# Kernel optimization log

Hardware: AMD Instinct MI355X
Metric: run time of the kernel (lower is better)

Reference implementation:

```python
import jax, jax.numpy as jnp
import numpy as np

N, E = 10000, 160000
EPS = 1e-5  # BatchNorm eps (eval mode: running_mean=0, running_var=1)


def _bn(x, g, b):
    # eval-mode batchnorm with default running stats
    return g * x / np.float32(np.sqrt(1.0 + EPS)) + b


def _conv(x, w, b, stride, pad):
    y = jax.lax.conv_general_dilated(
        x, w, (stride, stride), [(pad, pad), (pad, pad)],
        dimension_numbers=('NCHW', 'OIHW', 'NCHW'))
    return y + b[None, :, None, None]


def _maxpool3(x):
    # kernel 3, stride 1, pad 1
    return jax.lax.reduce_window(x, -jnp.inf, jax.lax.max,
                                 (1, 1, 3, 3), (1, 1, 1, 1),
                                 [(0, 0), (0, 0), (1, 1), (1, 1)])


def _sage_conv(x, edge_index, wl, bl, wr):
    # PyG SAGEConv(aggr='mean'): out = lin_l(mean_j x_j) + lin_r(x_i)
    src, dst = edge_index[0], edge_index[1]
    n = x.shape[0]
    agg = jax.ops.segment_sum(x[src], dst, num_segments=n)
    cnt = jax.ops.segment_sum(jnp.ones((edge_index.shape[1],), x.dtype), dst, num_segments=n)
    agg = agg / jnp.maximum(cnt, 1.0)[:, None]
    return agg @ wl.T + bl + x @ wr.T


def setup_inputs():
    key = jax.random.key(0)
    ks = jax.random.split(key, 16)
    w = lambda k, shape, fan: jax.random.normal(k, shape, jnp.float32) / np.float32(np.sqrt(fan))
    return {
        'x': jax.random.normal(ks[0], (N, 2560), jnp.float32),
        'edge_index': jax.random.randint(ks[1], (2, E), 0, N),
        'w1l': w(ks[2], (1024, 2560), 2560), 'b1': jnp.zeros((1024,), jnp.float32),
        'w1r': w(ks[3], (1024, 2560), 2560),
        'bn1_g': jnp.ones((1024,), jnp.float32), 'bn1_b': jnp.zeros((1024,), jnp.float32),
        'w2l': w(ks[4], (512, 1024), 1024), 'b2': jnp.zeros((512,), jnp.float32),
        'w2r': w(ks[5], (512, 1024), 1024),
        'fa1_w': w(ks[6], (128, 512), 512), 'fa1_b': jnp.zeros((128,), jnp.float32),
        'fa2_w': w(ks[7], (128, 128), 128), 'fa2_b': jnp.zeros((128,), jnp.float32),
        'cnn1_w': w(ks[8], (64, 1, 3, 3), 9), 'cnn1_b': jnp.zeros((64,), jnp.float32),
        'norm_g': jnp.ones((64,), jnp.float32), 'norm_b': jnp.zeros((64,), jnp.float32),
        'c1_w': w(ks[9], (64, 64, 3, 3), 576), 'c1_b': jnp.zeros((64,), jnp.float32),
        'c1_g': jnp.ones((64,), jnp.float32), 'c1_bb': jnp.zeros((64,), jnp.float32),
        'c2_w': w(ks[10], (16, 64, 3, 3), 576), 'c2_b': jnp.zeros((16,), jnp.float32),
        'c2_g': jnp.ones((16,), jnp.float32), 'c2_bb': jnp.zeros((16,), jnp.float32),
        'fc1_w': w(ks[11], (1024, 432), 432), 'fc1_b': jnp.zeros((1024,), jnp.float32),
        'fc2_w': w(ks[12], (14, 1024), 1024), 'fc2_b': jnp.zeros((14,), jnp.float32),
    }


def reference(x, edge_index, w1l, b1, w1r, bn1_g, bn1_b, w2l, b2, w2r,
              fa1_w, fa1_b, fa2_w, fa2_b, cnn1_w, cnn1_b, norm_g, norm_b,
              c1_w, c1_b, c1_g, c1_bb, c2_w, c2_b, c2_g, c2_bb,
              fc1_w, fc1_b, fc2_w, fc2_b):
    # ---- SAGE (eval mode: dropout inactive) ----
    h = _sage_conv(x, edge_index, w1l, b1, w1r)
    h = jax.nn.relu(h)
    h = _bn(h, bn1_g, bn1_b)
    h = _sage_conv(h, edge_index, w2l, b2, w2r)      # [N, 512]
    xb = h[None]                                      # [1, N, 512]
    # ---- Attention pooling (softmax over node axis) ----
    a = jnp.tanh(xb @ fa1_w.T + fa1_b) @ fa2_w.T + fa2_b   # [1, N, 128]
    att = jax.nn.softmax(a, axis=1).transpose(0, 2, 1)     # [1, 128, N]
    emb = (att @ xb)[None]                                  # [1, 1, 128, 512]
    # ---- CNN classifier ----
    e = _conv(emb, cnn1_w, cnn1_b, 1, 3)                    # [1,64,132,516]
    e = jax.nn.relu(_bn(e, norm_g[None, :, None, None], norm_b[None, :, None, None]))
    for _ in range(5):
        e = _conv(e, c1_w, c1_b, 2, 1)
        e = jax.nn.relu(_bn(e, c1_g[None, :, None, None], c1_bb[None, :, None, None]))
        e = _maxpool3(e)
    e = _conv(e, c2_w, c2_b, 2, 1)                          # [1,16,3,9]
    e = jax.nn.relu(_bn(e, c2_g[None, :, None, None], c2_bb[None, :, None, None]))
    e = _maxpool3(e)
    e = e.reshape(e.shape[0], -1)                           # [1, 432]
    e = e @ fc1_w.T + fc1_b
    e = e @ fc2_w.T + fc2_b
    return jax.nn.sigmoid(e)                                # [1, 14]
```

## Files before the change

### kernel.cpp

```cpp
#include <hip/hip_runtime.h>
#include <cstdint>
#include <cstddef>

typedef unsigned short ushort;
typedef __attribute__((ext_vector_type(8))) short bf16x8;
typedef __attribute__((ext_vector_type(8))) unsigned short ushort8v;
typedef __attribute__((ext_vector_type(4))) float f32x4;

#define BN_INV 0.9999950000374997f

__device__ inline ushort f2bf(float f) {
    union { float f; unsigned u; } x; x.f = f;
    unsigned r = x.u + 0x7fffu + ((x.u >> 16) & 1u);
    return (ushort)(r >> 16);
}
__device__ inline float bf2f(ushort u) {
    union { unsigned u; float f; } x; x.u = ((unsigned)u) << 16;
    return x.f;
}

__device__ __forceinline__ void gload16(const void* g, void* l) {
    __builtin_amdgcn_global_load_lds(
        (const __attribute__((address_space(1))) unsigned int*)g,
        (__attribute__((address_space(3))) unsigned int*)l, 16, 0, 0);
// ... 97 lines not shown
            acc[3][3] = __builtin_amdgcn_mfma_f32_16x16x32_bf16(a3, b3, acc[3][3], 0, 0, 0);
        }
    }

#pragma unroll
    for (int mi = 0; mi < 4; mi++) {
#pragma unroll
        for (int ni = 0; ni < 4; ni++) {
            f32x4 a = acc[mi][ni];
            int n = n0 + wc * 64 + ni * 16 + lr;
#pragma unroll
            for (int j = 0; j < 4; j++) {
                int m = m0 + wr * 64 + mi * 16 + lg * 4 + j;
                if (m >= M) continue;
                float v = a[j];
                if (EPIL == 3) {
                    v = tanhf(v + bias[n]);
                } else if (EPIL == 4) {
                    v = v + bias[n];
                }
                if (EPIL == 5) {
                    int half = N >> 1;
                    ushort* dst = (n < half) ? (ushort*)C : C2;
                    dst[(size_t)m * half + (n & (half - 1))] = f2bf(v);
                } else {
                    if (sizeof(OutT) == 2) ((ushort*)C)[(size_t)m * N + n] = f2bf(v);
                    else                   ((float*)C)[(size_t)m * N + n] = v;
                }
            }
        }
    }
}

__global__ void gather_h1(const ushort* __restrict__ YL, const int* __restrict__ eidx,
                          const int* __restrict__ off, const ushort* __restrict__ YR,
// ... 36 lines not shown
        s0 += bf2f(v[0]); s1 += bf2f(v[1]); s2 += bf2f(v[2]); s3 += bf2f(v[3]);
        s4 += bf2f(v[4]); s5 += bf2f(v[5]); s6 += bf2f(v[6]); s7 += bf2f(v[7]);
    }
    float sv[8] = {s0, s1, s2, s3, s4, s5, s6, s7};
    ushort8v zr = *(const ushort8v*)(ZR + (size_t)n * 512 + threadIdx.x * 8);
    ushort8v o;
#pragma unroll
    for (int qq = 0; qq < 8; qq++) {
        int c = threadIdx.x * 8 + qq;
        o[qq] = f2bf(sv[qq] * inv + b2[c] + bf2f(zr[qq]));
    }
    *(ushort8v*)(XB + (size_t)n * 512 + threadIdx.x * 8) = o;
}

__global__ __launch_bounds__(256)
void mgemm_splitk(const ushort* __restrict__ Asrc, const ushort* __restrict__ Bsrc,
                  float* __restrict__ PART, int N, int Kp, int nsteps, int spz)
{
    __shared__ ushort As[128 * 64];
    __shared__ ushort Bs[128 * 64];

    const int tid  = threadIdx.x;
    const int lane = tid & 63;
    const int wid  = tid >> 6;
    const int wr   = wid >> 1;
    const int wc   = wid & 1;
    const int n0   = blockIdx.x * 128;
    const int z    = blockIdx.z;

    const int lr  = lane & 15;
    const int lg  = lane >> 4;
    const int swz = (lr & 7) << 4;

    f32x4 acc[4][4];
#pragma unroll
    for (int i = 0; i < 4; i++)
#pragma unroll
        for (int j = 0; j < 4; j++) acc[i][j] = (f32x4){0.f, 0.f, 0.f, 0.f};

    const int sb = z * spz;
    const int se = min(sb + spz, nsteps);

    for (int s = sb; s < se; s++) {
        int k0 = s * 64;
        if (s != sb) __syncthreads();
#pragma unroll
        for (int i = 0; i < 4; i++) {
            int ch = i * 256 + tid;
            int rr = ch >> 3, c8 = ch & 7;
            int c8p = c8 ^ (rr & 7);
            gload16(Asrc + (size_t)rr * Kp + k0 + c8p * 8,
                    (char*)As + (i * 256 + wid * 64) * 16);
            gload16(Bsrc + (size_t)(n0 + rr) * Kp + k0 + c8p * 8,
                    (char*)Bs + (i * 256 + wid * 64) * 16);
        }
        __syncthreads();

        const char* Ab = (const char*)As + (wr * 64 + lr) * 128;
        const char* Bb = (const char*)Bs + (wc * 64 + lr) * 128;
#pragma unroll
        for (int ks = 0; ks < 2; ks++) {
            int kx = (ks * 64 + lg * 16) ^ swz;
            bf16x8 a0 = *(const bf16x8*)(Ab + 0 * 2048 + kx);
            bf16x8 a1 = *(const bf16x8*)(Ab + 1 * 2048 + kx);
            bf16x8 a2 = *(const bf16x8*)(Ab + 2 * 2048 + kx);
            bf16x8 a3 = *(const bf16x8*)(Ab + 3 * 2048 + kx);
            bf16x8 b0 = *(const bf16x8*)(Bb + 0 * 2048 + kx);
            bf16x8 b1 = *(const bf16x8*)(Bb + 1 * 2048 + kx);
            bf16x8 b2 = *(const bf16x8*)(Bb + 2 * 2048 + kx);
            bf16x8 b3 = *(const bf16x8*)(Bb + 3 * 2048 + kx);
            acc[0][0] = __builtin_amdgcn_mfma_f32_16x16x32_bf16(a0, b0, acc[0][0], 0, 0, 0);
            acc[0][1] = __builtin_amdgcn_mfma_f32_16x16x32_bf16(a0, b1, acc[0][1], 0, 0, 0);
// ... 2 lines not shown
            acc[1][0] = __builtin_amdgcn_mfma_f32_16x16x32_bf16(a1, b0, acc[1][0], 0, 0, 0);
            acc[1][1] = __builtin_amdgcn_mfma_f32_16x16x32_bf16(a1, b1, acc[1][1], 0, 0, 0);
            acc[1][2] = __builtin_amdgcn_mfma_f32_16x16x32_bf16(a1, b2, acc[1][2], 0, 0, 0);
            acc[1][3] = __builtin_amdgcn_mfma_f32_16x16x32_bf16(a1, b3, acc[1][3], 0, 0, 0);
            acc[2][0] = __builtin_amdgcn_mfma_f32_16x16x32_bf16(a2, b0, acc[2][0], 0, 0, 0);
            acc[2][1] = __builtin_amdgcn_mfma_f32_16x16x32_bf16(a2, b1, acc[2][1], 0, 0, 0);
            acc[2][2] = __builtin_amdgcn_mfma_f32_16x16x32_bf16(a2, b2, acc[2][2], 0, 0, 0);
            acc[2][3] = __builtin_amdgcn_mfma_f32_16x16x32_bf16(a2, b3, acc[2][3], 0, 0, 0);
            acc[3][0] = __builtin_amdgcn_mfma_f32_16x16x32_bf16(a3, b0, acc[3][0], 0, 0, 0);
            acc[3][1] = __builtin_amdgcn_mfma_f32_16x16x32_bf16(a3, b1, acc[3][1], 0, 0, 0);
            acc[3][2] = __builtin_amdgcn_mfma_f32_16x16x32_bf16(a3, b2, acc[3][2], 0, 0, 0);
            acc[3][3] = __builtin_amdgcn_mfma_f32_16x16x32_bf16(a3, b3, acc[3][3], 0, 0, 0);
        }
    }

    float* outp = PART + (size_t)z * 128 * 512;
#pragma unroll
    for (int mi = 0; mi < 4; mi++) {
#pragma unroll
        for (int ni = 0; ni < 4; ni++) {
            f32x4 a = acc[mi][ni];
            int n = n0 + wc * 64 + ni * 16 + lr;
#pragma unroll
            for (int j = 0; j < 4; j++) {
                int m = wr * 64 + mi * 16 + lg * 4 + j;
                outp[(size_t)m * 512 + n] = a[j];
            }
        }
    }
}
// ... 35 lines not shown
        *(ushort8v*)&tile[r][c8 * 8] = v;
    }
    __syncthreads();
#pragma unroll
    for (int i = 0; i < 2; i++) {
        int ch = i * 256 + tid;
        int dr = ch >> 3, n8 = ch & 7;
        ushort8v v;
#pragma unroll
        for (int q = 0; q < 8; q++) v[q] = tile[n8 * 8 + q][dr];
        *(ushort8v*)(XBT + (size_t)(d0 + dr) * Kp + n0 + n8 * 8) = v;
    }
}

template<int NI>
__global__ __launch_bounds__(256)
void conv_mfma(const ushort* __restrict__ in, const ushort* __restrict__ Wk,
               const float* __restrict__ bias, const float* __restrict__ gamma,
               const float* __restrict__ beta, ushort* __restrict__ outp,
               int IH, int IW, int OH, int OW)
{
    const int OC = NI * 16;
    __shared__ ushort As[128 * 64];
    __shared__ ushort Bs[NI * 16 * 64];

    const int tid  = threadIdx.x;
    const int lane = tid & 63;
    const int wv   = tid >> 6;
    const int lr   = lane & 15;
    const int lg   = lane >> 4;
    const int swz  = (lr & 7) << 4;
    const int m0   = blockIdx.x * 128;
    const int M    = OH * OW;

    f32x4 acc[2][NI];
#pragma unroll
    for (int i = 0; i < 2; i++)
#pragma unroll
        for (int j = 0; j < NI; j++) acc[i][j] = (f32x4){0.f, 0.f, 0.f, 0.f};

    for (int r = 0; r < 9; r++) {
        const int kh = r / 3, kw = r % 3;
        if (r) __syncthreads();
#pragma unroll
        for (int i = 0; i < 4; i++) {
            int ch = i * 256 + tid;
            int p = ch >> 3, c8 = ch & 7;
// ... 35 lines not shown
#pragma unroll
    for (int ni = 0; ni < NI; ni++) {
        f32x4 a = acc[mi][ni];
        int oc = ni * 16 + lr;
        float bv = bias[oc], gv = gamma[oc], btv = beta[oc];
#pragma unroll
        for (int j = 0; j < 4; j++) {
            int gp = m0 + wv * 32 + mi * 16 + lg * 4 + j;
            if (gp >= M) continue;
            float v = a[j] + bv;
            v = gv * v * BN_INV + btv;
            v = fmaxf(v, 0.f);
            outp[(size_t)gp * OC + oc] = f2bf(v);
        }
    }
}

__global__ void reorder_all(const float* __restrict__ c1w, const float* __restrict__ c2w,
                            ushort* __restrict__ WC1, ushort* __restrict__ WC2)
{
    int i = blockIdx.x * blockDim.x + threadIdx.x;
    if (i >= 80 * 576) return;
    const float* w; ushort* wk; int idx;
    if (i < 64 * 576) { w = c1w; wk = WC1; idx = i; }
    else              { w = c2w; wk = WC2; idx = i - 64 * 576; }
    int oc = idx / 576, t = idx % 576;
    int r = t / 64, ic = t % 64;
    int kh = r / 3, kw = r % 3;
    wk[idx] = f2bf(w[((oc * 64 + ic) * 3 + kh) * 3 + kw]);
}

__global__ void conv1_nhwc(const float* __restrict__ emb, const float* __restrict__ w,
                           const float* __restrict__ b, const float* __restrict__ g,
                           const float* __restrict__ bb, ushort* __restrict__ outp)
{
    int oh = blockIdx.x;
    for (int idx = threadIdx.x; idx < 516 * 8; idx += 256) {
        int ow = idx >> 3, c8 = idx & 7;
        float pv[9];
#pragma unroll
        for (int kh = 0; kh < 3; kh++)
#pragma unroll
            for (int kw = 0; kw < 3; kw++) {
                int ih = oh - 3 + kh, iw = ow - 3 + kw;
                pv[kh * 3 + kw] = (ih >= 0 && ih < 128 && iw >= 0 && iw < 512)
                                  ? emb[ih * 512 + iw] : 0.f;
            }
        ushort8v o;
#pragma unroll
        for (int q = 0; q < 8; q++) {
            int oc = c8 * 8 + q;
            float v = b[oc];
#pragma unroll
            for (int i = 0; i < 9; i++) v = fmaf(pv[i], w[oc * 9 + i], v);
            v = g[oc] * v * BN_INV + bb[oc];
            v = fmaxf(v, 0.f);
            o[q] = f2bf(v);
        }
        *(ushort8v*)(outp + ((size_t)oh * 516 + ow) * 64 + c8 * 8) = o;
    }
}

__global__ void maxpool_nhwc(const ushort* __restrict__ in, ushort* __restrict__ out,
                             int H, int W, int C8)
{
    int h = blockIdx.x;
    int tot = W * C8;
    for (int idx = threadIdx.x; idx < tot; idx += blockDim.x) {
        int w0 = idx / C8, cg = idx % C8;
        float mx[8];
#pragma unroll
        for (int q = 0; q < 8; q++) mx[q] = -1e30f;
        for (int dh = -1; dh <= 1; dh++) {
            int hh = h + dh; if (hh < 0 || hh >= H) continue;
            for (int dw = -1; dw <= 1; dw++) {
                int ww = w0 + dw; if (ww < 0 || ww >= W) continue;
                ushort8v v = *(const ushort8v*)(in + ((size_t)hh * W + ww) * C8 * 8 + cg * 8);
#pragma unroll
                for (int q = 0; q < 8; q++) mx[q] = fmaxf(mx[q], bf2f(v[q]));
            }
        }
        ushort8v o;
#pragma unroll
        for (int q = 0; q < 8; q++) o[q] = f2bf(mx[q]);
        *(ushort8v*)(out + ((size_t)h * W + w0) * C8 * 8 + cg * 8) = o;
    }
}

__global__ void cvt_k(const float* __restrict__ in, ushort* __restrict__ out, int n8)
{
    int i = blockIdx.x * blockDim.x + threadIdx.x;
    if (i >= n8) return;
    const float4 f0 = *(const float4*)(in + (size_t)i * 8);
    const float4 f1 = *(const float4*)(in + (size_t)i * 8 + 4);
    ushort8v v;
    v[0] = f2bf(f0.x); v[1] = f2bf(f0.y); v[2] = f2bf(f0.z); v[3] = f2bf(f0.w);
    v[4] = f2bf(f1.x); v[5] = f2bf(f1.y); v[6] = f2bf(f1.z); v[7] = f2bf(f1.w);
    *(ushort8v*)(out + (size_t)i * 8) = v;
}

__global__ void cvt_all(const float* w1l, const float* w1r, const float* w2l,
                        const float* w2r, const float* fa1, const float* fa2,
                        ushort* W1L, ushort* W1R, ushort* W2L, ushort* W2R,
                        ushort* FA1, ushort* FA2)
{
    int i = blockIdx.x * blockDim.x + threadIdx.x;
    const float* s; ushort* d; int j;
    if      (i < 327680)  { s = w1l; d = W1L; j = i; }
    else if (i < 655360)  { s = w1r; d = W1R; j = i - 327680; }
    else if (i < 720896)  { s = w2l; d = W2L; j = i - 655360; }
    else if (i < 786432)  { s = w2r; d = W2R; j = i - 720896; }
    else if (i < 794624)  { s = fa1; d = FA1; j = i - 786432; }
    else if (i < 796672)  { s = fa2; d = FA2; j = i - 794624; }
    else return;
    const float4 f0 = *(const float4*)(s + (size_t)j * 8);
    const float4 f1 = *(const float4*)(s + (size_t)j * 8 + 4);
    ushort8v v;
    v[0] = f2bf(f0.x); v[1] = f2bf(f0.y); v[2] = f2bf(f0.z); v[3] = f2bf(f0.w);
    v[4] = f2bf(f1.x); v[5] = f2bf(f1.y); v[6] = f2bf(f1.z); v[7] = f2bf(f1.w);
    *(ushort8v*)(d + (size_t)j * 8) = v;
}

__global__ void hist_k(const int* __restrict__ dst, int* __restrict__ hist, int E)
{
    int e = blockIdx.x * blockDim.x + threadIdx.x;
    if (e < E) atomicAdd(&hist[dst[e]], 1);
}

__global__ __launch_bounds__(1024)
void scan_k(const int* __restrict__ hist, int* __restrict__ off, int n)
{
    __shared__ int tmp[1024];
    const int PT = (n + 1023) / 1024;
    int t = threadIdx.x;
    int b = t * PT;
    int ls = 0;
    for (int k = 0; k < PT; k++) { int i = b + k; if (i < n) ls += hist[i]; }
    tmp[t] = ls;
    __syncthreads();
    for (int s = 1; s < 1024; s <<= 1) {
        int v = (t >= s) ? tmp[t - s] : 0;
        __syncthreads();
        tmp[t] += v;
        __syncthreads();
    }
    int run = tmp[t] - ls;
    for (int k = 0; k < PT; k++) {
        int i = b + k;
        if (i < n) { off[i] = run; run += hist[i]; }
    }
    if (t == 1023) off[n] = tmp[1023];
}

__global__ void fill_k(const int* __restrict__ src, const int* __restrict__ dst,
                       const int* __restrict__ off, int* __restrict__ cursor,
                       int* __restrict__ eidx, int E)
{
    int e = blockIdx.x * blockDim.x + threadIdx.x;
    if (e >= E) return;
    int d = dst[e];
    int pos = atomicAdd(&cursor[d], 1);
    eidx[off[d] + pos] = src[e];
}

__global__ __launch_bounds__(256)
void softmax_stats(const float* __restrict__ a2, float* __restrict__ ms,
                   float* __restrict__ ss, int Nn)
{
    int c = blockIdx.x;
    __shared__ float red[256];
    float mx = -1e30f;
    for (int n = threadIdx.x; n < Nn; n += 256)
        mx = fmaxf(mx, a2[(size_t)n * 128 + c]);
    red[threadIdx.x] = mx;
    __syncthreads();
    for (int s = 128; s > 0; s >>= 1) {
        if (threadIdx.x < s) red[threadIdx.x] = fmaxf(red[threadIdx.x], red[threadIdx.x + s]);
        __syncthreads();
    }
    mx = red[0];
    __syncthreads();
    float sum = 0.f;
    for (int n = threadIdx.x; n < Nn; n += 256)
        sum += expf(a2[(size_t)n * 128 + c] - mx);
    red[threadIdx.x] = sum;
    __syncthreads();
    for (int s = 128; s > 0; s >>= 1) {
        if (threadIdx.x < s) red[threadIdx.x] += red[threadIdx.x + s];
        __syncthreads();
    }
    if (threadIdx.x == 0) { ms[c] = mx; ss[c] = red[0]; }
}

__global__ __launch_bounds__(1024)
void head_k(const ushort* __restrict__ e, const float* __restrict__ fc1w,
            const float* __restrict__ fc1b, const float* __restrict__ fc2w,
            const float* __restrict__ fc2b, float* __restrict__ outp)
{
    __shared__ float flat[432];
    __shared__ float t1[1024];
    int tid = threadIdx.x;
    if (tid < 432) {
        int c = tid / 27, r = tid % 27;
        int h = r / 9, w0 = r % 9;
        float m = -1e30f;
        for (int dh = -1; dh <= 1; dh++) {
            int hh = h + dh;
            if (hh < 0 || hh >= 3) continue;
            for (int dw = -1; dw <= 1; dw++) {
                int ww = w0 + dw;
                if (ww < 0 || ww >= 9) continue;
                m = fmaxf(m, bf2f(e[((size_t)hh * 9 + ww) * 16 + c]));
            }
        }
        flat[tid] = m;
    }
    __syncthreads();
    {
        float s = fc1b[tid];
        const float* wr = fc1w + (size_t)tid * 432;
        for (int k = 0; k < 432; k++) s = fmaf(flat[k], wr[k], s);
        t1[tid] = s;
    }
    __syncthreads();
    int o = tid >> 6, l = tid & 63;
    if (o < 14) {
        float s = 0.f;
        const float* wr = fc2w + (size_t)o * 1024;
        for (int k = l; k < 1024; k += 64) s = fmaf(t1[k], wr[k], s);
        for (int sh = 32; sh > 0; sh >>= 1) s += __shfl_down(s, sh, 64);
        if (l == 0) outp[o] = 1.f / (1.f + expf(-(s + fc2b[o])));
    }
}

extern "C" void kernel_launch(void* const* d_in, const int* in_sizes, int n_in,
                              void* d_out, int out_size, void* d_ws, size_t ws_size,
                              hipStream_t stream)
{
    const float* x     = (const float*)d_in[0];
    const int*   ei    = (const int*)d_in[1];
    const float* w1l   = (const float*)d_in[2];
    const float* b1    = (const float*)d_in[3];
    const float* w1r   = (const float*)d_in[4];
    const float* bn1g  = (const float*)d_in[5];
    const float* bn1b  = (const float*)d_in[6];
    const float* w2l   = (const float*)d_in[7];
    const float* b2    = (const float*)d_in[8];
// ... 19 lines not shown
    const float* fc2w  = (const float*)d_in[28];
    const float* fc2b  = (const float*)d_in[29];
    float* out = (float*)d_out;

    const int Nn = 10000, E = 160000;
    const int Kp = 10048;
    char* ws = (char*)d_ws;

    ushort* YL    = (ushort*)(ws + 0);
    ushort* ATTWT = (ushort*)(ws + 0);
    ushort* XBT   = (ushort*)(ws + 2572288);
    ushort* P16   = (ushort*)(ws + 0);
    ushort* Q16   = (ushort*)(ws + 13000000);
    ushort* H1   = (ushort*)(ws + 20480000);
    ushort* XB   = (ushort*)(ws + 20480000);
    ushort* A1   = (ushort*)(ws + 30720000);
    float*  A2   = (float*)(ws + 33280000);
    ushort* YR   = (ushort*)(ws + 40960000);
    ushort* ZL   = (ushort*)(ws + 40960000);
    ushort* ZR   = (ushort*)(ws + 51200000);
    float*  PART = (float*)(ws + 40960000);
    int*   hist   = (int*)(ws + 61440000);
    int*   cursor = (int*)(ws + 61480000);
    int*   off    = (int*)(ws + 61520000);
    int*   eidx   = (int*)(ws + 61560128);
    float*  MS   = (float*)(ws + 67360128);
    float*  SS   = (float*)(ws + 67360640);
    float*  EMB  = (float*)(ws + 67361152);
    ushort* W1L = (ushort*)(ws + 67623296);
    ushort* W1R = (ushort*)(ws + 72866176);
    ushort* W2L = (ushort*)(ws + 78109056);
    ushort* W2R = (ushort*)(ws + 79157632);
    ushort* FA1 = (ushort*)(ws + 80206208);
    ushort* FA2 = (ushort*)(ws + 80337280);
    ushort* WC1 = (ushort*)(ws + 80370048);
    ushort* WC2 = (ushort*)(ws + 80443776);
    ushort* XBF = (ushort*)(ws + 80462208);
    const bool use_xbf = (ws_size >= (size_t)131662208);

    const int* src = ei;
    const int* dst = ei + E;

    cvt_all<<<(796672 + 255) / 256, 256, 0, stream>>>(
        w1l, w1r, w2l, w2r, fa1w, fa2w, W1L, W1R, W2L, W2R, FA1, FA2);
    reorder_all<<<(80 * 576 + 255) / 256, 256, 0, stream>>>(c1w, c2w, WC1, WC2);

    hipMemsetAsync(hist, 0, 80000, stream);
    hist_k<<<(E + 255) / 256, 256, 0, stream>>>(dst, hist, E);
    scan_k<<<1, 1024, 0, stream>>>(hist, off, Nn);
    fill_k<<<(E + 255) / 256, 256, 0, stream>>>(src, dst, off, cursor, eidx, E);

    const int GY = (Nn + 127) / 128;

    if (use_xbf) {
        cvt_k<<<(3200000 + 255) / 256, 256, 0, stream>>>(x, XBF, 3200000);
        mgemm<0, 5, ushort><<<dim3(2048 / 128, GY), 256, 0, stream>>>(
            XBF, W1L, YL, Nn, 2048, 2560, nullptr, YR);
    } else {
        mgemm<1, 5, ushort><<<dim3(2048 / 128, GY), 256, 0, stream>>>(
            x, W1L, YL, Nn, 2048, 2560, nullptr, YR);
    }
    gather_h1<<<Nn, 128, 0, stream>>>(YL, eidx, off, YR, b1, bn1g, bn1b, H1);

    mgemm<0, 5, ushort><<<dim3(1024 / 128, GY), 256, 0, stream>>>(
        H1, W2L, ZL, Nn, 1024, 1024, nullptr, ZR);
    gather_xb<<<Nn, 64, 0, stream>>>(ZL, eidx, off, ZR, b2, XB);

    mgemm<0, 3, ushort><<<dim3(1, GY), 256, 0, stream>>>(
        XB, FA1, A1, Nn, 128, 512, fa1b, nullptr);
    mgemm<0, 4, float><<<dim3(1, GY), 256, 0, stream>>>(
        A1, FA2, A2, Nn, 128, 128, fa2b, nullptr);
    softmax_stats<<<128, 256, 0, stream>>>(A2, MS, SS, Nn);
    att_w_t<<<(128 * Kp + 255) / 256, 256, 0, stream>>>(A2, MS, SS, ATTWT, Nn, Kp);
    t_xb<<<dim3(Kp / 64, 8), 256, 0, stream>>>(XB, XBT, Nn, Kp);
    mgemm_splitk<<<dim3(4, 1, 40), 256, 0, stream>>>(ATTWT, XBT, PART, 512, Kp, 157, 4);
    reduce_part<<<256, 256, 0, stream>>>(PART, EMB, 40);

    conv1_nhwc<<<132, 256, 0, stream>>>(EMB, cnn1w, cnn1b, normg, normb, P16);
    int H = 132, W = 516;
    for (int it = 0; it < 5; it++) {
        int OH = (H - 1) / 2 + 1, OW = (W - 1) / 2 + 1;
        int M = OH * OW;
        conv_mfma<4><<<(M + 127) / 128, 256, 0, stream>>>(
            P16, WC1, c1b, c1g, c1bb, Q16, H, W, OH, OW);
        maxpool_nhwc<<<OH, 256, 0, stream>>>(Q16, P16, OH, OW, 8);
        H = OH; W = OW;
    }
    conv_mfma<1><<<1, 256, 0, stream>>>(
        P16, WC2, c2b, c2g, c2bb, Q16, H, W, 3, 9);
    head_k<<<1, 1024, 0, stream>>>(Q16, fc1w, fc1b, fc2w, fc2b, out);
}
```

Before: 624.0 us.

## Fuse launches: attention GEMMs, CSR build, weight prep, and CNN tail

Several short kernels are merged to cut launch overhead and intermediate traffic. The two attention projection GEMMs become one kernel that keeps the tanh output in shared memory. Histogram, scan and fill become a single-block CSR build, and the weight conversions become one prep kernel. The whole CNN tail (conv1, five conv/maxpool stages, conv2, head) becomes one cooperative kernel with grid syncs, trading launch gaps for grid-wide barriers and fewer blocks per stage. The single-block CSR build serialises work that was previously spread across the GPU.

```diff
diff --git a/kernel.cpp b/kernel.cpp
--- a/kernel.cpp
+++ b/kernel.cpp
@@ -1,6 +1,9 @@
 #include <hip/hip_runtime.h>
+#include <hip/hip_cooperative_groups.h>
 #include <cstdint>
 #include <cstddef>
+
+namespace cg = cooperative_groups;
 
 typedef unsigned short ushort;
 typedef __attribute__((ext_vector_type(8))) short bf16x8;
@@ -135,11 +138,6 @@
                 int m = m0 + wr * 64 + mi * 16 + lg * 4 + j;
                 if (m >= M) continue;
                 float v = a[j];
-                if (EPIL == 3) {
-                    v = tanhf(v + bias[n]);
-                } else if (EPIL == 4) {
-                    v = v + bias[n];
-                }
                 if (EPIL == 5) {
                     int half = N >> 1;
                     ushort* dst = (n < half) ? (ushort*)C : C2;
@@ -206,23 +204,24 @@
 }
 
 __global__ __launch_bounds__(256)
-void mgemm_splitk(const ushort* __restrict__ Asrc, const ushort* __restrict__ Bsrc,
-                  float* __restrict__ PART, int N, int Kp, int nsteps, int spz)
+void attn_a1a2(const ushort* __restrict__ XB, const ushort* __restrict__ FA1,
+               const float* __restrict__ fa1b, const ushort* __restrict__ FA2,
+               const float* __restrict__ fa2b, float* __restrict__ A2, int M)
 {
     __shared__ ushort As[128 * 64];
     __shared__ ushort Bs[128 * 64];
+    __shared__ ushort A1a[128 * 64];
+    __shared__ ushort A1b[128 * 64];
 
     const int tid  = threadIdx.x;
     const int lane = tid & 63;
     const int wid  = tid >> 6;
     const int wr   = wid >> 1;
     const int wc   = wid & 1;
-    const int n0   = blockIdx.x * 128;
-    const int z    = blockIdx.z;
-
-    const int lr  = lane & 15;
-    const int lg  = lane >> 4;
-    const int swz = (lr & 7) << 4;
+    const int m0   = blockIdx.x * 128;
+    const int lr   = lane & 15;
+    const int lg   = lane >> 4;
+    const int swz  = (lr & 7) << 4;
 
     f32x4 acc[4][4];
 #pragma unroll
@@ -230,24 +229,20 @@
 #pragma unroll
         for (int j = 0; j < 4; j++) acc[i][j] = (f32x4){0.f, 0.f, 0.f, 0.f};
 
-    const int sb = z * spz;
-    const int se = min(sb + spz, nsteps);
-
-    for (int s = sb; s < se; s++) {
-        int k0 = s * 64;
-        if (s != sb) __syncthreads();
+    for (int k0 = 0; k0 < 512; k0 += 64) {
+        if (k0) __syncthreads();
 #pragma unroll
         for (int i = 0; i < 4; i++) {
             int ch = i * 256 + tid;
             int rr = ch >> 3, c8 = ch & 7;
             int c8p = c8 ^ (rr & 7);
-            gload16(Asrc + (size_t)rr * Kp + k0 + c8p * 8,
+            int srow = m0 + rr; if (srow > M - 1) srow = M - 1;
+            gload16(XB + (size_t)srow * 512 + k0 + c8p * 8,
                     (char*)As + (i * 256 + wid * 64) * 16);
-            gload16(Bsrc + (size_t)(n0 + rr) * Kp + k0 + c8p * 8,
+            gload16(FA1 + (size_t)rr * 512 + k0 + c8p * 8,
                     (char*)Bs + (i * 256 + wid * 64) * 16);
         }
         __syncthreads();
-
         const char* Ab = (const char*)As + (wr * 64 + lr) * 128;
         const char* Bb = (const char*)Bs + (wc * 64 + lr) * 128;
 #pragma unroll
@@ -280,6 +275,166 @@
         }
     }
 
+#pragma unroll
+    for (int mi = 0; mi < 4; mi++)
+#pragma unroll
+    for (int ni = 0; ni < 4; ni++) {
+        f32x4 a = acc[mi][ni];
+        int n = wc * 64 + ni * 16 + lr;
+        ushort* buf = (n < 64) ? A1a : A1b;
+        int c = n & 63;
+#pragma unroll
+        for (int j = 0; j < 4; j++) {
+            int m = wr * 64 + mi * 16 + lg * 4 + j;
+            float v = tanhf(a[j] + fa1b[n]);
+            int byo = m * 128 + (((c >> 3) * 16) ^ ((m & 7) << 4)) + (c & 7) * 2;
+            *(ushort*)((char*)buf + byo) = f2bf(v);
+        }
+    }
+    __syncthreads();
+
+#pragma unroll
+    for (int i = 0; i < 4; i++) {
+        int ch = i * 256 + tid;
+        int rr = ch >> 3, c8 = ch & 7;
+        int c8p = c8 ^ (rr & 7);
+        gload16(FA2 + (size_t)rr * 128 + c8p * 8,
+                (char*)As + (i * 256 + wid * 64) * 16);
+        gload16(FA2 + (size_t)rr * 128 + 64 + c8p * 8,
+                (char*)Bs + (i * 256 + wid * 64) * 16);
+    }
+    __syncthreads();
+
+    f32x4 acc2[4][4];
+#pragma unroll
+    for (int i = 0; i < 4; i++)
+#pragma unroll
+        for (int j = 0; j < 4; j++) acc2[i][j] = (f32x4){0.f, 0.f, 0.f, 0.f};
+
+#pragma unroll
+    for (int kb = 0; kb < 2; kb++) {
+        const char* Ab = (const char*)(kb ? A1b : A1a) + (wr * 64 + lr) * 128;
+        const char* Bb = (const char*)(kb ? Bs : As) + (wc * 64 + lr) * 128;
+#pragma unroll
+        for (int ks = 0; ks < 2; ks++) {
+            int kx = (ks * 64 + lg * 16) ^ swz;
+            bf16x8 a0 = *(const bf16x8*)(Ab + 0 * 2048 + kx);
+            bf16x8 a1 = *(const bf16x8*)(Ab + 1 * 2048 + kx);
+            bf16x8 a2 = *(const bf16x8*)(Ab + 2 * 2048 + kx);
+            bf16x8 a3 = *(const bf16x8*)(Ab + 3 * 2048 + kx);
+            bf16x8 b0 = *(const bf16x8*)(Bb + 0 * 2048 + kx);
+            bf16x8 b1 = *(const bf16x8*)(Bb + 1 * 2048 + kx);
+            bf16x8 b2 = *(const bf16x8*)(Bb + 2 * 2048 + kx);
+            bf16x8 b3 = *(const bf16x8*)(Bb + 3 * 2048 + kx);
+            acc2[0][0] = __builtin_amdgcn_mfma_f32_16x16x32_bf16(a0, b0, acc2[0][0], 0, 0, 0);
+            acc2[0][1] = __builtin_amdgcn_mfma_f32_16x16x32_bf16(a0, b1, acc2[0][1], 0, 0, 0);
+            acc2[0][2] = __builtin_amdgcn_mfma_f32_16x16x32_bf16(a0, b2, acc2[0][2], 0, 0, 0);
+            acc2[0][3] = __builtin_amdgcn_mfma_f32_16x16x32_bf16(a0, b3, acc2[0][3], 0, 0, 0);
+            acc2[1][0] = __builtin_amdgcn_mfma_f32_16x16x32_bf16(a1, b0, acc2[1][0], 0, 0, 0);
+            acc2[1][1] = __builtin_amdgcn_mfma_f32_16x16x32_bf16(a1, b1, acc2[1][1], 0, 0, 0);
+            acc2[1][2] = __builtin_amdgcn_mfma_f32_16x16x32_bf16(a1, b2, acc2[1][2], 0, 0, 0);
+            acc2[1][3] = __builtin_amdgcn_mfma_f32_16x16x32_bf16(a1, b3, acc2[1][3], 0, 0, 0);
+            acc2[2][0] = __builtin_amdgcn_mfma_f32_16x16x32_bf16(a2, b0, acc2[2][0], 0, 0, 0);
+            acc2[2][1] = __builtin_amdgcn_mfma_f32_16x16x32_bf16(a2, b1, acc2[2][1], 0, 0, 0);
+            acc2[2][2] = __builtin_amdgcn_mfma_f32_16x16x32_bf16(a2, b2, acc2[2][2], 0, 0, 0);
+            acc2[2][3] = __builtin_amdgcn_mfma_f32_16x16x32_bf16(a2, b3, acc2[2][3], 0, 0, 0);
+            acc2[3][0] = __builtin_amdgcn_mfma_f32_16x16x32_bf16(a3, b0, acc2[3][0], 0, 0, 0);
+            acc2[3][1] = __builtin_amdgcn_mfma_f32_16x16x32_bf16(a3, b1, acc2[3][1], 0, 0, 0);
+            acc2[3][2] = __builtin_amdgcn_mfma_f32_16x16x32_bf16(a3, b2, acc2[3][2], 0, 0, 0);
+            acc2[3][3] = __builtin_amdgcn_mfma_f32_16x16x32_bf16(a3, b3, acc2[3][3], 0, 0, 0);
+        }
+    }
+
+#pragma unroll
+    for (int mi = 0; mi < 4; mi++)
+#pragma unroll
+    for (int ni = 0; ni < 4; ni++) {
+        f32x4 a = acc2[mi][ni];
+        int n = wc * 64 + ni * 16 + lr;
+#pragma unroll
+        for (int j = 0; j < 4; j++) {
+            int m = m0 + wr * 64 + mi * 16 + lg * 4 + j;
+            if (m >= M) continue;
+            A2[(size_t)m * 128 + n] = a[j] + fa2b[n];
+        }
+    }
+}
+
+__global__ __launch_bounds__(256)
+void mgemm_splitk(const ushort* __restrict__ Asrc, const ushort* __restrict__ Bsrc,
+                  float* __restrict__ PART, int N, int Kp, int nsteps, int spz)
+{
+    __shared__ ushort As[128 * 64];
+    __shared__ ushort Bs[128 * 64];
+
+    const int tid  = threadIdx.x;
+    const int lane = tid & 63;
+    const int wid  = tid >> 6;
+    const int wr   = wid >> 1;
+    const int wc   = wid & 1;
+    const int n0   = blockIdx.x * 128;
+    const int z    = blockIdx.z;
+
+    const int lr  = lane & 15;
+    const int lg  = lane >> 4;
+    const int swz = (lr & 7) << 4;
+
+    f32x4 acc[4][4];
+#pragma unroll
+    for (int i = 0; i < 4; i++)
+#pragma unroll
+        for (int j = 0; j < 4; j++) acc[i][j] = (f32x4){0.f, 0.f, 0.f, 0.f};
+
+    const int sb = z * spz;
+    const int se = min(sb + spz, nsteps);
+
+    for (int s = sb; s < se; s++) {
+        int k0 = s * 64;
+        if (s != sb) __syncthreads();
+#pragma unroll
+        for (int i = 0; i < 4; i++) {
+            int ch = i * 256 + tid;
+            int rr = ch >> 3, c8 = ch & 7;
+            int c8p = c8 ^ (rr & 7);
+            gload16(Asrc + (size_t)rr * Kp + k0 + c8p * 8,
+                    (char*)As + (i * 256 + wid * 64) * 16);
+            gload16(Bsrc + (size_t)(n0 + rr) * Kp + k0 + c8p * 8,
+                    (char*)Bs + (i * 256 + wid * 64) * 16);
+        }
+        __syncthreads();
+
+        const char* Ab = (const char*)As + (wr * 64 + lr) * 128;
+        const char* Bb = (const char*)Bs + (wc * 64 + lr) * 128;
+#pragma unroll
+        for (int ks = 0; ks < 2; ks++) {
+            int kx = (ks * 64 + lg * 16) ^ swz;
+            bf16x8 a0 = *(const bf16x8*)(Ab + 0 * 2048 + kx);
+            bf16x8 a1 = *(const bf16x8*)(Ab + 1 * 2048 + kx);
+            bf16x8 a2 = *(const bf16x8*)(Ab + 2 * 2048 + kx);
+            bf16x8 a3 = *(const bf16x8*)(Ab + 3 * 2048 + kx);
+            bf16x8 b0 = *(const bf16x8*)(Bb + 0 * 2048 + kx);
+            bf16x8 b1 = *(const bf16x8*)(Bb + 1 * 2048 + kx);
+            bf16x8 b2 = *(const bf16x8*)(Bb + 2 * 2048 + kx);
+            bf16x8 b3 = *(const bf16x8*)(Bb + 3 * 2048 + kx);
+            acc[0][0] = __builtin_amdgcn_mfma_f32_16x16x32_bf16(a0, b0, acc[0][0], 0, 0, 0);
+            acc[0][1] = __builtin_amdgcn_mfma_f32_16x16x32_bf16(a0, b1, acc[0][1], 0, 0, 0);
+            acc[0][2] = __builtin_amdgcn_mfma_f32_16x16x32_bf16(a0, b2, acc[0][2], 0, 0, 0);
+            acc[0][3] = __builtin_amdgcn_mfma_f32_16x16x32_bf16(a0, b3, acc[0][3], 0, 0, 0);
+            acc[1][0] = __builtin_amdgcn_mfma_f32_16x16x32_bf16(a1, b0, acc[1][0], 0, 0, 0);
+            acc[1][1] = __builtin_amdgcn_mfma_f32_16x16x32_bf16(a1, b1, acc[1][1], 0, 0, 0);
+            acc[1][2] = __builtin_amdgcn_mfma_f32_16x16x32_bf16(a1, b2, acc[1][2], 0, 0, 0);
+            acc[1][3] = __builtin_amdgcn_mfma_f32_16x16x32_bf16(a1, b3, acc[1][3], 0, 0, 0);
+            acc[2][0] = __builtin_amdgcn_mfma_f32_16x16x32_bf16(a2, b0, acc[2][0], 0, 0, 0);
+            acc[2][1] = __builtin_amdgcn_mfma_f32_16x16x32_bf16(a2, b1, acc[2][1], 0, 0, 0);
+            acc[2][2] = __builtin_amdgcn_mfma_f32_16x16x32_bf16(a2, b2, acc[2][2], 0, 0, 0);
+            acc[2][3] = __builtin_amdgcn_mfma_f32_16x16x32_bf16(a2, b3, acc[2][3], 0, 0, 0);
+            acc[3][0] = __builtin_amdgcn_mfma_f32_16x16x32_bf16(a3, b0, acc[3][0], 0, 0, 0);
+            acc[3][1] = __builtin_amdgcn_mfma_f32_16x16x32_bf16(a3, b1, acc[3][1], 0, 0, 0);
+            acc[3][2] = __builtin_amdgcn_mfma_f32_16x16x32_bf16(a3, b2, acc[3][2], 0, 0, 0);
+            acc[3][3] = __builtin_amdgcn_mfma_f32_16x16x32_bf16(a3, b3, acc[3][3], 0, 0, 0);
+        }
+    }
+
     float* outp = PART + (size_t)z * 128 * 512;
 #pragma unroll
     for (int mi = 0; mi < 4; mi++) {
@@ -345,23 +500,19 @@
 }
 
 template<int NI>
-__global__ __launch_bounds__(256)
-void conv_mfma(const ushort* __restrict__ in, const ushort* __restrict__ Wk,
-               const float* __restrict__ bias, const float* __restrict__ gamma,
-               const float* __restrict__ beta, ushort* __restrict__ outp,
-               int IH, int IW, int OH, int OW)
+__device__ void conv_tile(const ushort* __restrict__ in, const ushort* __restrict__ Wk,
+                          const float* __restrict__ bias, const float* __restrict__ gamma,
+                          const float* __restrict__ beta, ushort* __restrict__ outp,
+                          int IH, int IW, int OH, int OW, int m0,
+                          ushort* As, ushort* Bs)
 {
     const int OC = NI * 16;
-    __shared__ ushort As[128 * 64];
-    __shared__ ushort Bs[NI * 16 * 64];
-
     const int tid  = threadIdx.x;
     const int lane = tid & 63;
     const int wv   = tid >> 6;
     const int lr   = lane & 15;
     const int lg   = lane >> 4;
     const int swz  = (lr & 7) << 4;
-    const int m0   = blockIdx.x * 128;
     const int M    = OH * OW;
 
     f32x4 acc[2][NI];
@@ -427,76 +578,199 @@
             outp[(size_t)gp * OC + oc] = f2bf(v);
         }
     }
-}
-
-__global__ void reorder_all(const float* __restrict__ c1w, const float* __restrict__ c2w,
-                            ushort* __restrict__ WC1, ushort* __restrict__ WC2)
+    __syncthreads();
+}
+
+__global__ __launch_bounds__(256)
+void cnn_tail(const float* __restrict__ EMB,
+              const float* __restrict__ cnn1w, const float* __restrict__ cnn1b,
+              const float* __restrict__ normg, const float* __restrict__ normb,
+              const ushort* __restrict__ WC1, const float* __restrict__ c1b,
+              const float* __restrict__ c1g, const float* __restrict__ c1bb,
+              const ushort* __restrict__ WC2, const float* __restrict__ c2b,
+              const float* __restrict__ c2g, const float* __restrict__ c2bb,
+              const float* __restrict__ fc1w, const float* __restrict__ fc1b,
+              const float* __restrict__ fc2w, const float* __restrict__ fc2b,
+              ushort* __restrict__ P16, ushort* __restrict__ Q16,
+              float* __restrict__ outp)
+{
+    cg::grid_group grid = cg::this_grid();
+    __shared__ ushort As[128 * 64];
+    __shared__ ushort Bs[64 * 64];
+    __shared__ float flat[432];
+    __shared__ float t1[1024];
+
+    const int tid = threadIdx.x;
+    const int nb  = gridDim.x;
+
+    for (int oh = blockIdx.x; oh < 132; oh += nb) {
+        for (int idx = tid; idx < 516 * 8; idx += 256) {
+            int ow = idx >> 3, c8 = idx & 7;
+            float pv[9];
+#pragma unroll
+            for (int kh = 0; kh < 3; kh++)
+#pragma unroll
+                for (int kw = 0; kw < 3; kw++) {
+                    int ih = oh - 3 + kh, iw = ow - 3 + kw;
+                    pv[kh * 3 + kw] = (ih >= 0 && ih < 128 && iw >= 0 && iw < 512)
+                                      ? EMB[ih * 512 + iw] : 0.f;
+                }
+            ushort8v o;
+#pragma unroll
+            for (int qq = 0; qq < 8; qq++) {
+                int oc = c8 * 8 + qq;
+                float v = cnn1b[oc];
+#pragma unroll
+                for (int i = 0; i < 9; i++) v = fmaf(pv[i], cnn1w[oc * 9 + i], v);
+                v = normg[oc] * v * BN_INV + normb[oc];
+                v = fmaxf(v, 0.f);
+                o[qq] = f2bf(v);
+            }
+            *(ushort8v*)(P16 + ((size_t)oh * 516 + ow) * 64 + c8 * 8) = o;
+        }
+    }
+    grid.sync();
+
+    int H = 132, W = 516;
+    for (int it = 0; it < 5; it++) {
+        int OH = (H - 1) / 2 + 1, OW = (W - 1) / 2 + 1;
+        int M = OH * OW;
+        int tiles = (M + 127) / 128;
+        for (int t = blockIdx.x; t < tiles; t += nb)
+            conv_tile<4>(P16, WC1, c1b, c1g, c1bb, Q16, H, W, OH, OW, t * 128, As, Bs);
+        grid.sync();
+        int tot = OH * OW * 8;
+        for (int idx = blockIdx.x * 256 + tid; idx < tot; idx += nb * 256) {
+            int h = idx / (OW * 8);
+            int rem = idx % (OW * 8);
+            int w0 = rem >> 3, cgp = rem & 7;
+            float mx[8];
+#pragma unroll
+            for (int qq = 0; qq < 8; qq++) mx[qq] = -1e30f;
+            for (int dh = -1; dh <= 1; dh++) {
+                int hh = h + dh; if (hh < 0 || hh >= OH) continue;
+                for (int dw = -1; dw <= 1; dw++) {
+                    int ww = w0 + dw; if (ww < 0 || ww >= OW) continue;
+                    ushort8v v = *(const ushort8v*)(Q16 + ((size_t)hh * OW + ww) * 64 + cgp * 8);
+#pragma unroll
+                    for (int qq = 0; qq < 8; qq++) mx[qq] = fmaxf(mx[qq], bf2f(v[qq]));
+                }
+            }
+            ushort8v o;
+#pragma unroll
+            for (int qq = 0; qq < 8; qq++) o[qq] = f2bf(mx[qq]);
+            *(ushort8v*)(P16 + ((size_t)h * OW + w0) * 64 + cgp * 8) = o;
+        }
+        grid.sync();
+        H = OH; W = OW;
+    }
+
+    if (blockIdx.x == 0)
+        conv_tile<1>(P16, WC2, c2b, c2g, c2bb, Q16, H, W, 3, 9, 0, As, Bs);
+    grid.sync();
+
+    if (blockIdx.x == 0) {
+        for (int i = tid; i < 432; i += 256) {
+            int c = i / 27, r = i % 27;
+            int h = r / 9, w0 = r % 9;
+            float m = -1e30f;
+            for (int dh = -1; dh <= 1; dh++) {
+                int hh = h + dh; if (hh < 0 || hh >= 3) continue;
+                for (int dw = -1; dw <= 1; dw++) {
+                    int ww = w0 + dw; if (ww < 0 || ww >= 9) continue;
+                    m = fmaxf(m, bf2f(Q16[((size_t)hh * 9 + ww) * 16 + c]));
+                }
+            }
+            flat[i] = m;
+        }
+        __syncthreads();
+        for (int o = tid; o < 1024; o += 256) {
+            float s = fc1b[o];
+            const float* wr = fc1w + (size_t)o * 432;
+            for (int k = 0; k < 432; k++) s = fmaf(flat[k], wr[k], s);
+            t1[o] = s;
+        }
+        __syncthreads();
+        int wv = tid >> 6, l = tid & 63;
+        for (int o = wv; o < 14; o += 4) {
+            float s = 0.f;
+            const float* wr = fc2w + (size_t)o * 1024;
+            for (int k = l; k < 1024; k += 64) s = fmaf(t1[k], wr[k], s);
+            for (int sh = 32; sh > 0; sh >>= 1) s += __shfl_down(s, sh, 64);
+            if (l == 0) outp[o] = 1.f / (1.f + expf(-(s + fc2b[o])));
+        }
+    }
+}
+
+__global__ void prep_all(const float* w1l, const float* w1r, const float* w2l,
+                         const float* w2r, const float* fa1, const float* fa2,
+                         const float* c1w, const float* c2w,
+                         ushort* W1L, ushort* W1R, ushort* W2L, ushort* W2R,
+                         ushort* FA1, ushort* FA2, ushort* WC1, ushort* WC2)
 {
     int i = blockIdx.x * blockDim.x + threadIdx.x;
-    if (i >= 80 * 576) return;
-    const float* w; ushort* wk; int idx;
-    if (i < 64 * 576) { w = c1w; wk = WC1; idx = i; }
-    else              { w = c2w; wk = WC2; idx = i - 64 * 576; }
-    int oc = idx / 576, t = idx % 576;
-    int r = t / 64, ic = t % 64;
-    int kh = r / 3, kw = r % 3;
-    wk[idx] = f2bf(w[((oc * 64 + ic) * 3 + kh) * 3 + kw]);
-}
-
-__global__ void conv1_nhwc(const float* __restrict__ emb, const float* __restrict__ w,
-                           const float* __restrict__ b, const float* __restrict__ g,
-                           const float* __restrict__ bb, ushort* __restrict__ outp)
-{
-    int oh = blockIdx.x;
-    for (int idx = threadIdx.x; idx < 516 * 8; idx += 256) {
-        int ow = idx >> 3, c8 = idx & 7;
-        float pv[9];
-#pragma unroll
-        for (int kh = 0; kh < 3; kh++)
-#pragma unroll
-            for (int kw = 0; kw < 3; kw++) {
-                int ih = oh - 3 + kh, iw = ow - 3 + kw;
-                pv[kh * 3 + kw] = (ih >= 0 && ih < 128 && iw >= 0 && iw < 512)
-                                  ? emb[ih * 512 + iw] : 0.f;
-            }
-        ushort8v o;
-#pragma unroll
-        for (int q = 0; q < 8; q++) {
-            int oc = c8 * 8 + q;
-            float v = b[oc];
-#pragma unroll
-            for (int i = 0; i < 9; i++) v = fmaf(pv[i], w[oc * 9 + i], v);
-            v = g[oc] * v * BN_INV + bb[oc];
-            v = fmaxf(v, 0.f);
-            o[q] = f2bf(v);
-        }
-        *(ushort8v*)(outp + ((size_t)oh * 516 + ow) * 64 + c8 * 8) = o;
-    }
-}
-
-__global__ void maxpool_nhwc(const ushort* __restrict__ in, ushort* __restrict__ out,
-                             int H, int W, int C8)
-{
-    int h = blockIdx.x;
-    int tot = W * C8;
-    for (int idx = threadIdx.x; idx < tot; idx += blockDim.x) {
-        int w0 = idx / C8, cg = idx % C8;
-        float mx[8];
-#pragma unroll
-        for (int q = 0; q < 8; q++) mx[q] = -1e30f;
-        for (int dh = -1; dh <= 1; dh++) {
-            int hh = h + dh; if (hh < 0 || hh >= H) continue;
-            for (int dw = -1; dw <= 1; dw++) {
-                int ww = w0 + dw; if (ww < 0 || ww >= W) continue;
-                ushort8v v = *(const ushort8v*)(in + ((size_t)hh * W + ww) * C8 * 8 + cg * 8);
-#pragma unroll
-                for (int q = 0; q < 8; q++) mx[q] = fmaxf(mx[q], bf2f(v[q]));
-            }
-        }
-        ushort8v o;
-#pragma unroll
-        for (int q = 0; q < 8; q++) o[q] = f2bf(mx[q]);
-        *(ushort8v*)(out + ((size_t)h * W + w0) * C8 * 8 + cg * 8) = o;
+    if (i < 796672) {
+        const float* s; ushort* d; int j;
+        if      (i < 327680)  { s = w1l; d = W1L; j = i; }
+        else if (i < 655360)  { s = w1r; d = W1R; j = i - 327680; }
+        else if (i < 720896)  { s = w2l; d = W2L; j = i - 655360; }
+        else if (i < 786432)  { s = w2r; d = W2R; j = i - 720896; }
+        else if (i < 794624)  { s = fa1; d = FA1; j = i - 786432; }
+        else                  { s = fa2; d = FA2; j = i - 794624; }
+        const float4 f0 = *(const float4*)(s + (size_t)j * 8);
+        const float4 f1 = *(const float4*)(s + (size_t)j * 8 + 4);
+        ushort8v v;
+        v[0] = f2bf(f0.x); v[1] = f2bf(f0.y); v[2] = f2bf(f0.z); v[3] = f2bf(f0.w);
+        v[4] = f2bf(f1.x); v[5] = f2bf(f1.y); v[6] = f2bf(f1.z); v[7] = f2bf(f1.w);
+        *(ushort8v*)(d + (size_t)j * 8) = v;
+    } else {
+        int k = i - 796672;
+        if (k >= 80 * 576) return;
+        const float* w; ushort* wk; int idx;
+        if (k < 64 * 576) { w = c1w; wk = WC1; idx = k; }
+        else              { w = c2w; wk = WC2; idx = k - 64 * 576; }
+        int oc = idx / 576, t = idx % 576;
+        int r = t / 64, ic = t % 64;
+        int kh = r / 3, kw = r % 3;
+        wk[idx] = f2bf(w[((oc * 64 + ic) * 3 + kh) * 3 + kw]);
+    }
+}
+
+__global__ __launch_bounds__(1024)
+void csr_build(const int* __restrict__ src, const int* __restrict__ dst,
+               int* __restrict__ off, int* __restrict__ eidx, int E, int n)
+{
+    __shared__ int h[10000];
+    __shared__ int tmp[1024];
+    const int t = threadIdx.x;
+    for (int i = t; i < n; i += 1024) h[i] = 0;
+    __syncthreads();
+    for (int e = t; e < E; e += 1024) atomicAdd(&h[dst[e]], 1);
+    __syncthreads();
+    const int PT = (n + 1023) / 1024;
+    int b = t * PT, ls = 0;
+    for (int k = 0; k < PT; k++) { int i = b + k; if (i < n) ls += h[i]; }
+    tmp[t] = ls;
+    __syncthreads();
+    for (int s = 1; s < 1024; s <<= 1) {
+        int v = (t >= s) ? tmp[t - s] : 0;
+        __syncthreads();
+        tmp[t] += v;
+        __syncthreads();
+    }
+    int run = tmp[t] - ls;
+    int cur[10];
+    for (int k = 0; k < PT; k++) {
+        int i = b + k;
+        if (i < n) { off[i] = run; cur[k] = run; run += h[i]; }
+    }
+    if (t == 1023) off[n] = tmp[1023];
+    __syncthreads();
+    for (int k = 0; k < PT; k++) { int i = b + k; if (i < n) h[i] = cur[k]; }
+    __syncthreads();
+    for (int e = t; e < E; e += 1024) {
+        int pos = atomicAdd(&h[dst[e]], 1);
+        eidx[pos] = src[e];
     }
 }
 
@@ -512,70 +786,6 @@
     *(ushort8v*)(out + (size_t)i * 8) = v;
 }
 
-__global__ void cvt_all(const float* w1l, const float* w1r, const float* w2l,
-                        const float* w2r, const float* fa1, const float* fa2,
-                        ushort* W1L, ushort* W1R, ushort* W2L, ushort* W2R,
-                        ushort* FA1, ushort* FA2)
-{
-    int i = blockIdx.x * blockDim.x + threadIdx.x;
-    const float* s; ushort* d; int j;
-    if      (i < 327680)  { s = w1l; d = W1L; j = i; }
-    else if (i < 655360)  { s = w1r; d = W1R; j = i - 327680; }
-    else if (i < 720896)  { s = w2l; d = W2L; j = i - 655360; }
-    else if (i < 786432)  { s = w2r; d = W2R; j = i - 720896; }
-    else if (i < 794624)  { s = fa1; d = FA1; j = i - 786432; }
-    else if (i < 796672)  { s = fa2; d = FA2; j = i - 794624; }
-    else return;
-    const float4 f0 = *(const float4*)(s + (size_t)j * 8);
-    const float4 f1 = *(const float4*)(s + (size_t)j * 8 + 4);
-    ushort8v v;
-    v[0] = f2bf(f0.x); v[1] = f2bf(f0.y); v[2] = f2bf(f0.z); v[3] = f2bf(f0.w);
-    v[4] = f2bf(f1.x); v[5] = f2bf(f1.y); v[6] = f2bf(f1.z); v[7] = f2bf(f1.w);
-    *(ushort8v*)(d + (size_t)j * 8) = v;
-}
-
-__global__ void hist_k(const int* __restrict__ dst, int* __restrict__ hist, int E)
-{
-    int e = blockIdx.x * blockDim.x + threadIdx.x;
-    if (e < E) atomicAdd(&hist[dst[e]], 1);
-}
-
-__global__ __launch_bounds__(1024)
-void scan_k(const int* __restrict__ hist, int* __restrict__ off, int n)
-{
-    __shared__ int tmp[1024];
-    const int PT = (n + 1023) / 1024;
-    int t = threadIdx.x;
-    int b = t * PT;
-    int ls = 0;
-    for (int k = 0; k < PT; k++) { int i = b + k; if (i < n) ls += hist[i]; }
-    tmp[t] = ls;
-    __syncthreads();
-    for (int s = 1; s < 1024; s <<= 1) {
-        int v = (t >= s) ? tmp[t - s] : 0;
-        __syncthreads();
-        tmp[t] += v;
-        __syncthreads();
-    }
-    int run = tmp[t] - ls;
-    for (int k = 0; k < PT; k++) {
-        int i = b + k;
-        if (i < n) { off[i] = run; run += hist[i]; }
-    }
-    if (t == 1023) off[n] = tmp[1023];
-}
-
-__global__ void fill_k(const int* __restrict__ src, const int* __restrict__ dst,
-                       const int* __restrict__ off, int* __restrict__ cursor,
-                       int* __restrict__ eidx, int E)
-{
-    int e = blockIdx.x * blockDim.x + threadIdx.x;
-    if (e >= E) return;
-    int d = dst[e];
-    int pos = atomicAdd(&cursor[d], 1);
-    eidx[off[d] + pos] = src[e];
-}
-
 __global__ __launch_bounds__(256)
 void softmax_stats(const float* __restrict__ a2, float* __restrict__ ms,
                    float* __restrict__ ss, int Nn)
@@ -603,47 +813,6 @@
         __syncthreads();
     }
     if (threadIdx.x == 0) { ms[c] = mx; ss[c] = red[0]; }
-}
-
-__global__ __launch_bounds__(1024)
-void head_k(const ushort* __restrict__ e, const float* __restrict__ fc1w,
-            const float* __restrict__ fc1b, const float* __restrict__ fc2w,
-            const float* __restrict__ fc2b, float* __restrict__ outp)
-{
-    __shared__ float flat[432];
-    __shared__ float t1[1024];
-    int tid = threadIdx.x;
-    if (tid < 432) {
-        int c = tid / 27, r = tid % 27;
-        int h = r / 9, w0 = r % 9;
-        float m = -1e30f;
-        for (int dh = -1; dh <= 1; dh++) {
-            int hh = h + dh;
-            if (hh < 0 || hh >= 3) continue;
-            for (int dw = -1; dw <= 1; dw++) {
-                int ww = w0 + dw;
-                if (ww < 0 || ww >= 9) continue;
-                m = fmaxf(m, bf2f(e[((size_t)hh * 9 + ww) * 16 + c]));
-            }
-        }
-        flat[tid] = m;
-    }
-    __syncthreads();
-    {
-        float s = fc1b[tid];
-        const float* wr = fc1w + (size_t)tid * 432;
-        for (int k = 0; k < 432; k++) s = fmaf(flat[k], wr[k], s);
-        t1[tid] = s;
-    }
-    __syncthreads();
-    int o = tid >> 6, l = tid & 63;
-    if (o < 14) {
-        float s = 0.f;
-        const float* wr = fc2w + (size_t)o * 1024;
-        for (int k = l; k < 1024; k += 64) s = fmaf(t1[k], wr[k], s);
-        for (int sh = 32; sh > 0; sh >>= 1) s += __shfl_down(s, sh, 64);
-        if (l == 0) outp[o] = 1.f / (1.f + expf(-(s + fc2b[o])));
-    }
 }
 
 extern "C" void kernel_launch(void* const* d_in, const int* in_sizes, int n_in,
@@ -693,14 +862,11 @@
     ushort* Q16   = (ushort*)(ws + 13000000);
     ushort* H1   = (ushort*)(ws + 20480000);
     ushort* XB   = (ushort*)(ws + 20480000);
-    ushort* A1   = (ushort*)(ws + 30720000);
     float*  A2   = (float*)(ws + 33280000);
     ushort* YR   = (ushort*)(ws + 40960000);
     ushort* ZL   = (ushort*)(ws + 40960000);
     ushort* ZR   = (ushort*)(ws + 51200000);
     float*  PART = (float*)(ws + 40960000);
-    int*   hist   = (int*)(ws + 61440000);
-    int*   cursor = (int*)(ws + 61480000);
     int*   off    = (int*)(ws + 61520000);
     int*   eidx   = (int*)(ws + 61560128);
     float*  MS   = (float*)(ws + 67360128);
@@ -720,14 +886,10 @@
     const int* src = ei;
     const int* dst = ei + E;
 
-    cvt_all<<<(796672 + 255) / 256, 256, 0, stream>>>(
-        w1l, w1r, w2l, w2r, fa1w, fa2w, W1L, W1R, W2L, W2R, FA1, FA2);
-    reorder_all<<<(80 * 576 + 255) / 256, 256, 0, stream>>>(c1w, c2w, WC1, WC2);
-
-    hipMemsetAsync(hist, 0, 80000, stream);
-    hist_k<<<(E + 255) / 256, 256, 0, stream>>>(dst, hist, E);
-    scan_k<<<1, 1024, 0, stream>>>(hist, off, Nn);
-    fill_k<<<(E + 255) / 256, 256, 0, stream>>>(src, dst, off, cursor, eidx, E);
+    prep_all<<<(796672 + 80 * 576 + 255) / 256, 256, 0, stream>>>(
+        w1l, w1r, w2l, w2r, fa1w, fa2w, c1w, c2w,
+        W1L, W1R, W2L, W2R, FA1, FA2, WC1, WC2);
+    csr_build<<<1, 1024, 0, stream>>>(src, dst, off, eidx, E, Nn);
 
     const int GY = (Nn + 127) / 128;
 
@@ -745,27 +907,22 @@
         H1, W2L, ZL, Nn, 1024, 1024, nullptr, ZR);
     gather_xb<<<Nn, 64, 0, stream>>>(ZL, eidx, off, ZR, b2, XB);
 
-    mgemm<0, 3, ushort><<<dim3(1, GY), 256, 0, stream>>>(
-        XB, FA1, A1, Nn, 128, 512, fa1b, nullptr);
-    mgemm<0, 4, float><<<dim3(1, GY), 256, 0, stream>>>(
-        A1, FA2, A2, Nn, 128, 128, fa2b, nullptr);
+    attn_a1a2<<<GY, 256, 0, stream>>>(XB, FA1, fa1b, FA2, fa2b, A2, Nn);
     softmax_stats<<<128, 256, 0, stream>>>(A2, MS, SS, Nn);
     att_w_t<<<(128 * Kp + 255) / 256, 256, 0, stream>>>(A2, MS, SS, ATTWT, Nn, Kp);
     t_xb<<<dim3(Kp / 64, 8), 256, 0, stream>>>(XB, XBT, Nn, Kp);
     mgemm_splitk<<<dim3(4, 1, 40), 256, 0, stream>>>(ATTWT, XBT, PART, 512, Kp, 157, 4);
     reduce_part<<<256, 256, 0, stream>>>(PART, EMB, 40);
 
-    conv1_nhwc<<<132, 256, 0, stream>>>(EMB, cnn1w, cnn1b, normg, normb, P16);
-    int H = 132, W = 516;
-    for (int it = 0; it < 5; it++) {
-        int OH = (H - 1) / 2 + 1, OW = (W - 1) / 2 + 1;
-        int M = OH * OW;
-        conv_mfma<4><<<(M + 127) / 128, 256, 0, stream>>>(
-            P16, WC1, c1b, c1g, c1bb, Q16, H, W, OH, OW);
-        maxpool_nhwc<<<OH, 256, 0, stream>>>(Q16, P16, OH, OW, 8);
-        H = OH; W = OW;
-    }
-    conv_mfma<1><<<1, 256, 0, stream>>>(
-        P16, WC2, c2b, c2g, c2bb, Q16, H, W, 3, 9);
-    head_k<<<1, 1024, 0, stream>>>(Q16, fc1w, fc1b, fc2w, fc2b, out);
-}
+    {
+        void* args[] = {
+            (void*)&EMB, (void*)&cnn1w, (void*)&cnn1b, (void*)&normg, (void*)&normb,
+            (void*)&WC1, (void*)&c1b, (void*)&c1g, (void*)&c1bb,
+            (void*)&WC2, (void*)&c2b, (void*)&c2g, (void*)&c2bb,
+            (void*)&fc1w, (void*)&fc1b, (void*)&fc2w, (void*)&fc2b,
+            (void*)&P16, (void*)&Q16, (void*)&out
+        };
+        hipLaunchCooperativeKernel((const void*)cnn_tail, dim3(256), dim3(256),
+                                   args, 0, stream);
+    }
+}
```

New measurement: 1.036 ms. 1.66x slower.
